# Kernel optimization log

Hardware: AMD Instinct MI355X
Metric: run time of the kernel (lower is better)

## Reference

```python
import jax, jax.numpy as jnp
import numpy as np
from jax import lax

B, L, D, H = 2, 2048, 2048, 16
DH = D // H            # 128 head dim
D_REL = 64             # relevance projection dim (class const)
K = max(1, int(0.25 * L))  # top-K_FRAC tokens per query
NEG_INF = float('-inf')


def setup_inputs() -> dict:
    key = jax.random.key(0)
    ks = jax.random.split(key, 8)
    s = D ** (-0.5)
    return {
        'hidden_states': jax.random.normal(ks[0], (B, L, D), jnp.float32),
        'relevance':     jax.random.normal(ks[1], (B, L, D), jnp.float32),
        # torch nn.Linear weights are [out_features, in_features]
        'W_q_rel': jax.random.normal(ks[2], (D_REL, D), jnp.float32) * s,
        'W_k_rel': jax.random.normal(ks[3], (D_REL, D), jnp.float32) * s,
        'W_q': jax.random.normal(ks[4], (D, D), jnp.float32) * s,
        'W_k': jax.random.normal(ks[5], (D, D), jnp.float32) * s,
        'W_v': jax.random.normal(ks[6], (D, D), jnp.float32) * s,
        'W_o': jax.random.normal(ks[7], (D, D), jnp.float32) * s,
    }


def _rel_scores(relevance, W_q_rel, W_k_rel):
    # low-rank relevance logits, causally masked: [B, L, L]
    q = relevance @ W_q_rel.T   # [B, L, d_rel]
    k = relevance @ W_k_rel.T   # [B, L, d_rel]
    scores = jnp.einsum('bqd,bkd->bqk', q, k) * (D_REL ** -0.5)
    future = jnp.triu(jnp.ones((L, L), dtype=bool), k=1)
    return jnp.where(future[None], NEG_INF, scores)


def _sparse_mask(rel_scores):
    # additive mask [B, 1, L, L]: top-k per query row -> 0.0, else -inf; diag 0.0
    _, topk_idx = lax.top_k(rel_scores, K)            # [B, L, K]
    b = jnp.arange(B)[:, None, None]
    q = jnp.arange(L)[None, :, None]
    mask = jnp.full((B, L, L), NEG_INF, dtype=rel_scores.dtype)
    mask = mask.at[b, q, topk_idx].set(0.0)
    diag = jnp.arange(L)
    mask = mask.at[:, diag, diag].set(0.0)
    return mask[:, None]  # [B, 1, L, L]


def _attention(hidden_states, W_q, W_k, W_v, W_o, add_mask):
    # standard multi-head attention with additive mask (the wrapped frozen attn)
    q = (hidden_states @ W_q.T).reshape(B, L, H, DH)
    k = (hidden_states @ W_k.T).reshape(B, L, H, DH)
    v = (hidden_states @ W_v.T).reshape(B, L, H, DH)
    scores = jnp.einsum('bqhd,bkhd->bhqk', q, k) * (DH ** -0.5)
    scores = scores + add_mask                      # [B, H, L, L]
    p = jax.nn.softmax(scores, axis=-1)
    ctx = jnp.einsum('bhqk,bkhd->bqhd', p, v).reshape(B, L, D)
    return ctx @ W_o.T


def reference(hidden_states, relevance, W_q_rel, W_k_rel, W_q, W_k, W_v, W_o):
    # Phase 1 path (step >= SPARSE_FROM), no external attention_mask:
    # combined = causal(-inf upper-tri) + sparse top-k mask.
    rel = _rel_scores(relevance, W_q_rel, W_k_rel)
    sparse = _sparse_mask(rel)                      # [B, 1, L, L]
    future = jnp.triu(jnp.ones((L, L), dtype=bool), k=1)
    causal = jnp.where(future, NEG_INF, 0.0).astype(hidden_states.dtype)
    combined = causal[None, None] + sparse          # [B, 1, L, L]
    return _attention(hidden_states, W_q, W_k, W_v, W_o, combined)
```

## Files before the change

### kernel.cpp

```cpp
#include <hip/hip_runtime.h>
#include <math.h>
#include <stdint.h>

#define Bb 2
#define Lq 2048
#define Dm 2048
#define Hh 16
#define DH 128
#define DREL 64
#define KTOP 512

#define NEG_INF (-__builtin_huge_valf())

typedef __attribute__((ext_vector_type(8))) short bf16x8;
typedef __attribute__((ext_vector_type(4))) float f32x4;

static __device__ __forceinline__ unsigned short f2bf(float f) {
  unsigned int u = __float_as_uint(f);
  u += 0x7fffu + ((u >> 16) & 1u);
  return (unsigned short)(u >> 16);
}

static __device__ __forceinline__ void gload16(const void* g, void* lds) {
  __builtin_amdgcn_global_load_lds(
      (const __attribute__((address_space(1))) uint32_t*)(uintptr_t)g,
      (__attribute__((address_space(3))) uint32_t*)(uint32_t)(uintptr_t)lds,
      16, 0, 0);
}

__global__ __launch_bounds__(256) void conv_bf16(const float* __restrict__ in,
                                                 unsigned short* __restrict__ out,
                                                 int n8, float scale) {
  const int i = blockIdx.x * 256 + threadIdx.x;
  if (i >= n8) return;
  const float4 f0 = ((const float4*)in)[2 * i];
  const float4 f1 = ((const float4*)in)[2 * i + 1];
  bf16x8 o;
  o[0] = (short)f2bf(f0.x * scale); o[1] = (short)f2bf(f0.y * scale);
  o[2] = (short)f2bf(f0.z * scale); o[3] = (short)f2bf(f0.w * scale);
  o[4] = (short)f2bf(f1.x * scale); o[5] = (short)f2bf(f1.y * scale);
  o[6] = (short)f2bf(f1.z * scale); o[7] = (short)f2bf(f1.w * scale);
  *(bf16x8*)(out + 8 * (size_t)i) = o;
}

template <bool BF16OUT>
__global__ __launch_bounds__(256) void gemm_bf(const unsigned short* __restrict__ A,
                                               const unsigned short* __restrict__ W,
                                               void* __restrict__ Cv,
                                               int M, int N, int Kd) {
  __shared__ unsigned short As[128][32];
  __shared__ unsigned short Bs[128][32];
  const int tid = threadIdx.x;
  const int w = tid >> 6;
  const int lane = tid & 63;
  const int l15 = lane & 15;
  const int quad = lane >> 4;
  const int wm = w >> 1, wn = w & 1;
  const int m0 = blockIdx.y * 128, n0 = blockIdx.x * 128;

  const int srow = lane >> 2;
  const int scol = (lane & 3) * 8;

  const unsigned short* aR0 = A + (size_t)(m0 + w * 32 + srow) * Kd + scol;
  const unsigned short* aR1 = aR0 + (size_t)16 * Kd;
  const unsigned short* bR0 = W + (size_t)(n0 + w * 32 + srow) * Kd + scol;
  const unsigned short* bR1 = bR0 + (size_t)16 * Kd;

  f32x4 acc[4][4];
#pragma unroll
  for (int i = 0; i < 4; ++i)
#pragma unroll
    for (int j = 0; j < 4; ++j) acc[i][j] = (f32x4){0.f, 0.f, 0.f, 0.f};

  for (int k0 = 0; k0 < Kd; k0 += 32) {
    gload16(aR0 + k0, &As[w * 32][0]);
    gload16(aR1 + k0, &As[w * 32 + 16][0]);
    gload16(bR0 + k0, &Bs[w * 32][0]);
    gload16(bR1 + k0, &Bs[w * 32 + 16][0]);
    __syncthreads();

    bf16x8 af[4], bfr[4];
#pragma unroll
    for (int im = 0; im < 4; ++im)
      af[im] = *(const bf16x8*)&As[wm * 64 + im * 16 + l15][quad * 8];
#pragma unroll
    for (int in = 0; in < 4; ++in)
      bfr[in] = *(const bf16x8*)&Bs[wn * 64 + in * 16 + l15][quad * 8];
#pragma unroll
    for (int im = 0; im < 4; ++im)
#pragma unroll
      for (int in = 0; in < 4; ++in)
        acc[im][in] = __builtin_amdgcn_mfma_f32_16x16x32_bf16(af[im], bfr[in], acc[im][in], 0, 0, 0);
    __syncthreads();
  }

#pragma unroll
  for (int im = 0; im < 4; ++im) {
#pragma unroll
    for (int in = 0; in < 4; ++in) {
      const int col = n0 + wn * 64 + in * 16 + l15;
#pragma unroll
      for (int r = 0; r < 4; ++r) {
        const int row = m0 + wm * 64 + im * 16 + quad * 4 + r;
        if (BF16OUT)
          ((unsigned short*)Cv)[(size_t)row * N + col] = f2bf(acc[im][in][r]);
        else
          ((float*)Cv)[(size_t)row * N + col] = acc[im][in][r];
      }
    }
  }
}

#define RKS 8
__global__ __launch_bounds__(256) void relproj(const float* __restrict__ A,
                                               const float* __restrict__ W,
                                               float* __restrict__ part, int M) {
  __shared__ float As[16][128];
  __shared__ float Bs[16][64];
  const int ks = blockIdx.x;
  const int m0 = blockIdx.y * 128;
  const int tid = threadIdx.x;
  const int tx = tid & 15;
  const int ty = tid >> 4;
  const int lr = tid >> 1, lk = (tid & 1) * 8;
  const int wr = tid >> 2, wk = (tid & 3) * 4;

  float acc[8][4];
#pragma unroll
  for (int i = 0; i < 8; ++i)
#pragma unroll
    for (int j = 0; j < 4; ++j) acc[i][j] = 0.f;

  const int k00 = ks * (Dm / RKS);
  for (int k0 = k00; k0 < k00 + Dm / RKS; k0 += 16) {
    {
      const float* ap = A + (size_t)(m0 + lr) * Dm + k0 + lk;
      float4 a0 = *(const float4*)(ap);
      float4 a1 = *(const float4*)(ap + 4);
      As[lk + 0][lr] = a0.x; As[lk + 1][lr] = a0.y;
      As[lk + 2][lr] = a0.z; As[lk + 3][lr] = a0.w;
      As[lk + 4][lr] = a1.x; As[lk + 5][lr] = a1.y;
      As[lk + 6][lr] = a1.z; As[lk + 7][lr] = a1.w;
    }
    {
      const float* bp = W + (size_t)wr * Dm + k0 + wk;
      float4 b0 = *(const float4*)(bp);
      Bs[wk + 0][wr] = b0.x; Bs[wk + 1][wr] = b0.y;
      Bs[wk + 2][wr] = b0.z; Bs[wk + 3][wr] = b0.w;
    }
    __syncthreads();
#pragma unroll
    for (int kk = 0; kk < 16; ++kk) {
      float af[8], bf[4];
#pragma unroll
      for (int i = 0; i < 8; ++i) af[i] = As[kk][ty * 8 + i];
#pragma unroll
      for (int j = 0; j < 4; ++j) bf[j] = Bs[kk][tx * 4 + j];
#pragma unroll
      for (int i = 0; i < 8; ++i)
#pragma unroll
        for (int j = 0; j < 4; ++j) acc[i][j] += af[i] * bf[j];
    }
    __syncthreads();
  }

#pragma unroll
  for (int i = 0; i < 8; ++i) {
    float* pp = part + ((size_t)ks * M + m0 + ty * 8 + i) * DREL + tx * 4;
    *(float4*)pp = make_float4(acc[i][0], acc[i][1], acc[i][2], acc[i][3]);
  }
}

__global__ __launch_bounds__(256) void relreduce(const float* __restrict__ pq,
                                                 const float* __restrict__ pk,
                                                 float* __restrict__ qrel,
                                                 float* __restrict__ krel, int n4) {
  const int i = blockIdx.x * 256 + threadIdx.x;
  if (i >= n4) return;
  float4 sq = make_float4(0, 0, 0, 0), sk = sq;
  for (int s = 0; s < RKS; ++s) {
    float4 a = ((const float4*)pq)[(size_t)s * n4 + i];
    float4 b = ((const float4*)pk)[(size_t)s * n4 + i];
    sq.x += a.x; sq.y += a.y; sq.z += a.z; sq.w += a.w;
    sk.x += b.x; sk.y += b.y; sk.z += b.z; sk.w += b.w;
  }
  ((float4*)qrel)[i] = sq;
  ((float4*)krel)[i] = sk;
}

__global__ __launch_bounds__(256) void relscore(const float* __restrict__ qrel,
                                                const float* __restrict__ krel,
                                                float* __restrict__ S) {
  const int jt = blockIdx.x, qt = blockIdx.y, b = blockIdx.z;
  if (jt > qt) return;
  __shared__ float As[16][128];
  __shared__ float Bs[16][128];
  const int tid = threadIdx.x;
  const int q0 = qt * 128, j0 = jt * 128;
  const int tx = tid & 15, ty = tid >> 4;
  const int lr = tid >> 1, lk = (tid & 1) * 8;
  const float* Ab = qrel + (size_t)b * Lq * DREL;
  const float* Kb = krel + (size_t)b * Lq * DREL;

  float acc[8][8];
#pragma unroll
  for (int i = 0; i < 8; ++i)
#pragma unroll
    for (int j = 0; j < 8; ++j) acc[i][j] = 0.f;

  for (int k0 = 0; k0 < DREL; k0 += 16) {
    {
      const float* ap = Ab + (size_t)(q0 + lr) * DREL + k0 + lk;
      float4 a0 = *(const float4*)(ap);
      float4 a1 = *(const float4*)(ap + 4);
      As[lk + 0][lr] = a0.x; As[lk + 1][lr] = a0.y;
      As[lk + 2][lr] = a0.z; As[lk + 3][lr] = a0.w;
      As[lk + 4][lr] = a1.x; As[lk + 5][lr] = a1.y;
      As[lk + 6][lr] = a1.z; As[lk + 7][lr] = a1.w;
    }
    {
      const float* bp = Kb + (size_t)(j0 + lr) * DREL + k0 + lk;
      float4 b0 = *(const float4*)(bp);
      float4 b1 = *(const float4*)(bp + 4);
      Bs[lk + 0][lr] = b0.x; Bs[lk + 1][lr] = b0.y;
      Bs[lk + 2][lr] = b0.z; Bs[lk + 3][lr] = b0.w;
      Bs[lk + 4][lr] = b1.x; Bs[lk + 5][lr] = b1.y;
      Bs[lk + 6][lr] = b1.z; Bs[lk + 7][lr] = b1.w;
    }
    __syncthreads();
#pragma unroll
    for (int kk = 0; kk < 16; ++kk) {
      float af[8], bf[8];
#pragma unroll
      for (int i = 0; i < 8; ++i) af[i] = As[kk][ty * 8 + i];
#pragma unroll
      for (int j = 0; j < 8; ++j) bf[j] = Bs[kk][tx * 8 + j];
#pragma unroll
      for (int i = 0; i < 8; ++i)
#pragma unroll
        for (int j = 0; j < 8; ++j) acc[i][j] += af[i] * bf[j];
    }
    __syncthreads();
  }

  const float sc = 0.125f;
#pragma unroll
  for (int i = 0; i < 8; ++i) {
    float* cp = S + ((size_t)b * Lq + q0 + ty * 8 + i) * Lq + j0 + tx * 8;
    ((float4*)cp)[0] = make_float4(acc[i][0] * sc, acc[i][1] * sc, acc[i][2] * sc, acc[i][3] * sc);
    ((float4*)cp)[1] = make_float4(acc[i][4] * sc, acc[i][5] * sc, acc[i][6] * sc, acc[i][7] * sc);
  }
}

__global__ __launch_bounds__(256) void relselect(const float* __restrict__ S,
                                                 uint32_t* __restrict__ mask) {
  const int w = threadIdx.x >> 6;
  const int lane = threadIdx.x & 63;
  const int ridx = blockIdx.x * 4 + w;
  const int qi = ridx & (Lq - 1);
  const int n = qi + 1;
  const float* srow = S + (size_t)ridx * Lq;

  uint32_t keys[32];
#pragma unroll
  for (int t = 0; t < 32; ++t) {
    const int j = t * 64 + lane;
    const uint32_t u = __float_as_uint(srow[j]);
    const uint32_t k = (u & 0x80000000u) ? ~u : (u | 0x80000000u);
    keys[t] = (j < n) ? k : 0u;
  }

  uint32_t kth = 0u;
  if (n > KTOP) {
    uint32_t pref = 0u;
    int rem = KTOP;
    for (int bit = 31; bit >= 0; --bit) {
      const uint32_t cand = pref | (1u << bit);
      const uint32_t lim = 1u << bit;
      int c = 0;
#pragma unroll
      for (int t = 0; t < 32; ++t) c += ((keys[t] ^ cand) < lim) ? 1 : 0;
      c += __shfl_xor(c, 1);
      c += __shfl_xor(c, 2);
      c += __shfl_xor(c, 4);
      c += __shfl_xor(c, 8);
      c += __shfl_xor(c, 16);
      c += __shfl_xor(c, 32);
      if (c >= rem) pref = cand;
      else rem -= c;
    }
    kth = pref;
  }

  uint32_t* mrow = mask + (size_t)ridx * (Lq / 32);
#pragma unroll
  for (int t = 0; t < 32; ++t) {
    const int j = t * 64 + lane;
    const bool ok = (j < n) && (keys[t] >= kth || j == qi);
    const unsigned long long bal = __ballot(ok);
    if (lane == 0) {
      mrow[2 * t] = (uint32_t)bal;
      mrow[2 * t + 1] = (uint32_t)(bal >> 32);
    }
  }
}

#define ATQ 128
#define TK 64
__global__ __launch_bounds__(512, 4) void attn_flash3(const unsigned short* __restrict__ qkv,
                                                      const uint32_t* __restrict__ mask,
                                                      unsigned short* __restrict__ ctx) {
  __shared__ unsigned short Ks[2][TK][136];
  __shared__ unsigned short Vt[2][2][64][72];
  __shared__ uint32_t mw[2][ATQ][2];

  const int qt = (blockIdx.z == 0) ? ((Lq / ATQ) - 1 - (int)blockIdx.x) : (int)blockIdx.x;
  const int h = blockIdx.y;
  const int b = blockIdx.z;
  const int tid = threadIdx.x;
  const int w = tid >> 6;
  const int lane = tid & 63;
  const int l15 = lane & 15;
  const int quad = lane >> 4;
  const int q0 = qt * ATQ;
  const int STR = 3 * Dm;

  const unsigned short* kbp = qkv + 2048;
  const unsigned short* vbp = qkv + 4096;

  const int myq = q0 + w * 16 + l15;
  const unsigned short* qrow = qkv + (size_t)(b * Lq + myq) * STR + h * DH;
  bf16x8 bq[4];
#pragma unroll
  for (int kk = 0; kk < 4; ++kk) bq[kk] = *(const bf16x8*)(qrow + kk * 32 + quad * 8);

  f32x4 O[8];
#pragma unroll
  for (int f = 0; f < 8; ++f) O[f] = (f32x4){0.f, 0.f, 0.f, 0.f};
  float l_lane = 0.f;

  const int nt = (q0 + ATQ) / TK;

  const int skey = (tid & 255) >> 2;
  const int scg  = tid & 3;
  const int mq   = (tid & 255) >> 1;
  const int msel = tid & 1;
  const int tv = tid - 256;
  const int vkp = tv & 31;
  const int vdg = (tv >> 5) & 7;
  const int vhalf = vkp >> 4;
  const int vkp16 = vkp & 15;
  const int dwc = ((vkp16 >> 1) & 3) * 4 + (vkp16 >> 3) * 2 + (vkp16 & 1);

  const uint32_t* mrow_base = mask + (size_t)(b * Lq + q0 + mq) * (Lq / 32) + msel;
  const unsigned short* krow_base = kbp + (size_t)(b * Lq + skey) * STR + h * DH + scg * 32;
  const unsigned short* vrow_base = vbp + (size_t)(b * Lq + 2 * vkp) * STR + h * DH + vdg * 16;

  bf16x8 r0, r1, r2, r3;
  uint32_t mreg = 0;

#define LOADREGS(KT)                                                       \
  do {                                                                     \
    const int kbase_ = (KT) * TK;                                          \
    if (tid < 256) {                                                       \
      const unsigned short* kr = krow_base + (size_t)kbase_ * STR;         \
      r0 = *(const bf16x8*)(kr);                                           \
      r1 = *(const bf16x8*)(kr + 8);                                       \
      r2 = *(const bf16x8*)(kr + 16);                                      \
      r3 = *(const bf16x8*)(kr + 24);                                      \
      mreg = mrow_base[(KT) * 2];                                          \
    } else {                                                               \
      const unsigned short* vr = vrow_base + (size_t)kbase_ * STR;         \
      r0 = *(const bf16x8*)(vr);                                           \
      r1 = *(const bf16x8*)(vr + 8);                                       \
      r2 = *(const bf16x8*)(vr + STR);                                     \
      r3 = *(const bf16x8*)(vr + STR + 8);                                 \
    }                                                                      \
  } while (0)

#define WRITELDS(BUF)                                                      \
  do {                                                                     \
    if (tid < 256) {                                                       \
      *(bf16x8*)&Ks[BUF][skey][scg * 32 + 0]  = r0;                        \
      *(bf16x8*)&Ks[BUF][skey][scg * 32 + 8]  = r1;                        \
      *(bf16x8*)&Ks[BUF][skey][scg * 32 + 16] = r2;                        \
      *(bf16x8*)&Ks[BUF][skey][scg * 32 + 24] = r3;                        \
      mw[BUF][mq][msel] = mreg;                                            \
    } else {                                                               \
      _Pragma("unroll") for (int i = 0; i < 8; ++i) {                      \
        const int d = vdg * 16 + i;                                        \
        const uint32_t pk = (uint32_t)(unsigned short)r0[i] |              \
                            ((uint32_t)(unsigned short)r2[i] << 16);       \
        ((uint32_t*)&Vt[BUF][vhalf][d >> 1][0])[(d & 1) * 16 + dwc] = pk;  \
      }                                                                    \
      _Pragma("unroll") for (int i = 0; i < 8; ++i) {                      \
        const int d = vdg * 16 + 8 + i;                                    \
        const uint32_t pk = (uint32_t)(unsigned short)r1[i] |              \
                            ((uint32_t)(unsigned short)r3[i] << 16);       \
        ((uint32_t*)&Vt[BUF][vhalf][d >> 1][0])[(d & 1) * 16 + dwc] = pk;  \
      }                                                                    \
    }                                                                      \
  } while (0)

  LOADREGS(0);
  WRITELDS(0);
  __syncthreads();

  int buf = 0;
  for (int kt = 0; kt < nt; ++kt) {
    const bool more = (kt + 1 < nt);
    if (more) LOADREGS(kt + 1);

    __builtin_amdgcn_s_setprio(1);
#pragma unroll
    for (int hh = 0; hh < 2; ++hh) {
      f32x4 acc0 = (f32x4){0.f, 0.f, 0.f, 0.f};
      f32x4 acc1 = acc0;
#pragma unroll
      for (int kk = 0; kk < 4; ++kk) {
        bf16x8 a0 = *(const bf16x8*)&Ks[buf][hh * 32 + l15][kk * 32 + quad * 8];
        bf16x8 a1 = *(const bf16x8*)&Ks[buf][hh * 32 + 16 + l15][kk * 32 + quad * 8];
        acc0 = __builtin_amdgcn_mfma_f32_16x16x32_bf16(a0, bq[kk], acc0, 0, 0, 0);
        acc1 = __builtin_amdgcn_mfma_f32_16x16x32_bf16(a1, bq[kk], acc1, 0, 0, 0);
      }

      const uint32_t mword = mw[buf][w * 16 + l15][hh];
      bf16x8 bp;
      float ps = 0.f;
#pragma unroll
      for (int r = 0; r < 4; ++r) {
        const float p0 = ((mword >> (quad * 4 + r)) & 1u) ? __builtin_amdgcn_exp2f(acc0[r]) : 0.f;
        const float p1 = ((mword >> (16 + quad * 4 + r)) & 1u) ? __builtin_amdgcn_exp2f(acc1[r]) : 0.f;
        ps += p0 + p1;
        bp[r] = (short)f2bf(p0);
        bp[4 + r] = (short)f2bf(p1);
      }
      l_lane += ps;

#pragma unroll
      for (int f = 0; f < 8; ++f) {
        const int d = f * 16 + l15;
        bf16x8 av = *(const bf16x8*)&Vt[buf][hh][d >> 1][(d & 1) * 32 + quad * 8];
        O[f] = __builtin_amdgcn_mfma_f32_16x16x32_bf16(av, bp, O[f], 0, 0, 0);
      }
    }
    __builtin_amdgcn_s_setprio(0);

    if (more) WRITELDS(buf ^ 1);
    __syncthreads();
    buf ^= 1;
  }
#undef LOADREGS
#undef WRITELDS

  l_lane += __shfl_xor(l_lane, 16);
  l_lane += __shfl_xor(l_lane, 32);
  const float rl = 1.0f / l_lane;

  unsigned short* orow = ctx + ((size_t)(b * Lq + q0 + w * 16 + l15)) * Dm + h * DH;
#pragma unroll
  for (int f = 0; f < 8; ++f) {
    ushort4 o4;
    o4.x = f2bf(O[f][0] * rl);
    o4.y = f2bf(O[f][1] * rl);
    o4.z = f2bf(O[f][2] * rl);
    o4.w = f2bf(O[f][3] * rl);
    *(ushort4*)(orow + f * 16 + quad * 4) = o4;
  }
}

extern "C" void kernel_launch(void* const* d_in, const int* in_sizes, int n_in,
                              void* d_out, int out_size, void* d_ws, size_t ws_size,
                              hipStream_t stream) {
  const float* hs  = (const float*)d_in[0];
  const float* rel = (const float*)d_in[1];
  const float* Wqr = (const float*)d_in[2];
  const float* Wkr = (const float*)d_in[3];
  const float* Wq  = (const float*)d_in[4];
  const float* Wk  = (const float*)d_in[5];
  const float* Wv  = (const float*)d_in[6];
  const float* Wo  = (const float*)d_in[7];
  float* out = (float*)d_out;

  const int M = Bb * Lq;
  const int ND = Dm * Dm;
  char* ws = (char*)d_ws;
  size_t off = 0;
  float* qrel = (float*)(ws + off); off += (size_t)M * DREL * 4;
  float* krel = (float*)(ws + off); off += (size_t)M * DREL * 4;
  uint32_t* maskb = (uint32_t*)(ws + off); off += (size_t)M * (Lq / 32) * 4;
  float* partq = (float*)(ws + off); off += (size_t)RKS * M * DREL * 4;
  float* partk = (float*)(ws + off); off += (size_t)RKS * M * DREL * 4;
  float* Sbuf = (float*)(ws + off);
  unsigned short* hsb  = (unsigned short*)(ws + off); off += (size_t)M * Dm * 2;
  unsigned short* qkvb = (unsigned short*)(ws + off); off += (size_t)M * 3 * Dm * 2;
  unsigned short* ctxb = (unsigned short*)(ws + off); off += (size_t)M * Dm * 2;
  unsigned short* Wqb  = (unsigned short*)(ws + off); off += (size_t)ND * 2;
  unsigned short* Wkb  = (unsigned short*)(ws + off); off += (size_t)ND * 2;
  unsigned short* Wvb  = (unsigned short*)(ws + off); off += (size_t)ND * 2;
  unsigned short* Wob  = (unsigned short*)(ws + off); off += (size_t)ND * 2;

  const dim3 blk(256);
  const int hsN8 = M * Dm / 8;
  const int wN8  = ND / 8;
  const float QSCALE = 0.08838834764831845f * 1.4426950408889634f;

  relproj<<<dim3(RKS, M / 128), blk, 0, stream>>>(rel, Wqr, partq, M);
  relproj<<<dim3(RKS, M / 128), blk, 0, stream>>>(rel, Wkr, partk, M);
  relreduce<<<(M * DREL / 4 + 255) / 256, blk, 0, stream>>>(partq, partk, qrel, krel, M * DREL / 4);
  relscore<<<dim3(Lq / 128, Lq / 128, Bb), blk, 0, stream>>>(qrel, krel, Sbuf);
  relselect<<<M / 4, blk, 0, stream>>>(Sbuf, maskb);

  conv_bf16<<<(hsN8 + 255) / 256, blk, 0, stream>>>(hs, hsb, hsN8, 1.0f);
  conv_bf16<<<(wN8 + 255) / 256, blk, 0, stream>>>(Wq, Wqb, wN8, QSCALE);
  conv_bf16<<<(wN8 + 255) / 256, blk, 0, stream>>>(Wk, Wkb, wN8, 1.0f);
  conv_bf16<<<(wN8 + 255) / 256, blk, 0, stream>>>(Wv, Wvb, wN8, 1.0f);
  conv_bf16<<<(wN8 + 255) / 256, blk, 0, stream>>>(Wo, Wob, wN8, 1.0f);

  gemm_bf<true><<<dim3(3 * Dm / 128, M / 128), blk, 0, stream>>>(hsb, Wqb, qkvb, M, 3 * Dm, Dm);

  attn_flash3<<<dim3(Lq / ATQ, Hh, Bb), dim3(512), 0, stream>>>(qkvb, maskb, ctxb);

  gemm_bf<false><<<dim3(Dm / 128, M / 128), blk, 0, stream>>>(ctxb, Wob, out, M, Dm, Dm);
}
```

Baseline: 524.1 us.

## Replace GEMM with 256x256 double-buffered swizzled tile kernel and merge small launches

Replaces the 128x128 single-buffered bf16 GEMM with a 256x256-tile, 512-thread kernel. The new kernel double-buffers 64-wide K slices in LDS with an XOR swizzle, splits the MFMA work into phases with s_setprio, and remaps workgroup IDs in an XCD-aware order. It also merges the four weight-conversion launches into one and the two relevance-projection launches into one z-indexed launch. The aim is more data reuse per tile, less global-load latency exposure and bank conflicts, and less launch overhead. The cost is more registers and LDS per block, and fewer blocks for the output projection (128 tiles).

```diff
diff --git a/kernel.cpp b/kernel.cpp
--- a/kernel.cpp
+++ b/kernel.cpp
@@ -43,65 +43,153 @@
   *(bf16x8*)(out + 8 * (size_t)i) = o;
 }
 
+__global__ __launch_bounds__(256) void conv_bf16_w4(const float* __restrict__ w0,
+                                                    const float* __restrict__ w1,
+                                                    const float* __restrict__ w2,
+                                                    const float* __restrict__ w3,
+                                                    unsigned short* __restrict__ out,
+                                                    float s0) {
+  const int sel = blockIdx.y;
+  const float* in = (sel == 0) ? w0 : (sel == 1) ? w1 : (sel == 2) ? w2 : w3;
+  const float scale = (sel == 0) ? s0 : 1.0f;
+  const int i = blockIdx.x * 256 + threadIdx.x;
+  const float4 f0 = ((const float4*)in)[2 * i];
+  const float4 f1 = ((const float4*)in)[2 * i + 1];
+  bf16x8 o;
+  o[0] = (short)f2bf(f0.x * scale); o[1] = (short)f2bf(f0.y * scale);
+  o[2] = (short)f2bf(f0.z * scale); o[3] = (short)f2bf(f0.w * scale);
+  o[4] = (short)f2bf(f1.x * scale); o[5] = (short)f2bf(f1.y * scale);
+  o[6] = (short)f2bf(f1.z * scale); o[7] = (short)f2bf(f1.w * scale);
+  *(bf16x8*)(out + (size_t)sel * Dm * Dm + 8 * (size_t)i) = o;
+}
+
 template <bool BF16OUT>
-__global__ __launch_bounds__(256) void gemm_bf(const unsigned short* __restrict__ A,
-                                               const unsigned short* __restrict__ W,
-                                               void* __restrict__ Cv,
-                                               int M, int N, int Kd) {
-  __shared__ unsigned short As[128][32];
-  __shared__ unsigned short Bs[128][32];
+__global__ __launch_bounds__(512, 2) void gemm256(const unsigned short* __restrict__ A,
+                                                  const unsigned short* __restrict__ W,
+                                                  void* __restrict__ Cv,
+                                                  int M, int N, int Kd) {
+  __shared__ unsigned short As[2][2][128][64];
+  __shared__ unsigned short Bs[2][2][128][64];
+
   const int tid = threadIdx.x;
   const int w = tid >> 6;
   const int lane = tid & 63;
   const int l15 = lane & 15;
   const int quad = lane >> 4;
-  const int wm = w >> 1, wn = w & 1;
-  const int m0 = blockIdx.y * 128, n0 = blockIdx.x * 128;
-
-  const int srow = lane >> 2;
-  const int scol = (lane & 3) * 8;
-
-  const unsigned short* aR0 = A + (size_t)(m0 + w * 32 + srow) * Kd + scol;
-  const unsigned short* aR1 = aR0 + (size_t)16 * Kd;
-  const unsigned short* bR0 = W + (size_t)(n0 + w * 32 + srow) * Kd + scol;
-  const unsigned short* bR1 = bR0 + (size_t)16 * Kd;
-
-  f32x4 acc[4][4];
-#pragma unroll
-  for (int i = 0; i < 4; ++i)
+  const int wm = w >> 2;
+  const int wn = w & 3;
+
+  const int gx = N >> 8;
+  const int nwg = (M >> 8) * gx;
+  const int cpx = nwg >> 3;
+  const int bid = (int)blockIdx.x;
+  const int lin = (bid & 7) * cpx + (bid >> 3);
+  const int bx = lin % gx, by = lin / gx;
+  const int m0 = by * 256, n0 = bx * 256;
+
+  const int srow = lane >> 3;
+  const int sslot = (lane & 7) ^ srow;
+  const size_t rowK = (size_t)Kd;
+  const unsigned short* aG0 = A + (size_t)(m0 + w * 8 + srow) * rowK + sslot * 8;
+  const unsigned short* aG1 = aG0 + 64 * rowK;
+  const unsigned short* aG2 = aG0 + 128 * rowK;
+  const unsigned short* aG3 = aG0 + 192 * rowK;
+  const unsigned short* bG0 = W + (size_t)(n0 + w * 8 + srow) * rowK + sslot * 8;
+  const unsigned short* bG1 = bG0 + 64 * rowK;
+  const unsigned short* bG2 = bG0 + 128 * rowK;
+  const unsigned short* bG3 = bG0 + 192 * rowK;
+
+  f32x4 acc[8][4];
+#pragma unroll
+  for (int i = 0; i < 8; ++i)
 #pragma unroll
     for (int j = 0; j < 4; ++j) acc[i][j] = (f32x4){0.f, 0.f, 0.f, 0.f};
 
-  for (int k0 = 0; k0 < Kd; k0 += 32) {
-    gload16(aR0 + k0, &As[w * 32][0]);
-    gload16(aR1 + k0, &As[w * 32 + 16][0]);
-    gload16(bR0 + k0, &Bs[w * 32][0]);
-    gload16(bR1 + k0, &Bs[w * 32 + 16][0]);
+  bf16x8 af[4][2];
+  bf16x8 bfr[2][2];
+  const int swz = (l15 & 7) * 8;
+
+#define STAGE(BUF, T)                                         \
+  do {                                                        \
+    const size_t ko = (size_t)(T) * 64;                       \
+    gload16(aG0 + ko, &As[BUF][0][w * 8][0]);                 \
+    gload16(aG1 + ko, &As[BUF][0][64 + w * 8][0]);            \
+    gload16(aG2 + ko, &As[BUF][1][w * 8][0]);                 \
+    gload16(aG3 + ko, &As[BUF][1][64 + w * 8][0]);            \
+    gload16(bG0 + ko, &Bs[BUF][0][w * 8][0]);                 \
+    gload16(bG1 + ko, &Bs[BUF][0][64 + w * 8][0]);            \
+    gload16(bG2 + ko, &Bs[BUF][1][w * 8][0]);                 \
+    gload16(bG3 + ko, &Bs[BUF][1][64 + w * 8][0]);            \
+  } while (0)
+
+#define LOAD_A(BUF, MH)                                                        \
+  _Pragma("unroll") for (int mi = 0; mi < 4; ++mi)                             \
+    _Pragma("unroll") for (int ks = 0; ks < 2; ++ks)                           \
+      af[mi][ks] = *(const bf16x8*)&As[BUF][wm][(MH) * 64 + mi * 16 + l15]     \
+                                      [(ks * 32 + quad * 8) ^ swz];
+
+#define LOAD_B(BUF, NH)                                                        \
+  _Pragma("unroll") for (int ni = 0; ni < 2; ++ni)                             \
+    _Pragma("unroll") for (int ks = 0; ks < 2; ++ks)                           \
+      bfr[ni][ks] = *(const bf16x8*)&Bs[BUF][wn >> 1]                          \
+          [(wn & 1) * 64 + ((NH) * 2 + ni) * 16 + l15]                         \
+          [(ks * 32 + quad * 8) ^ swz];
+
+#define PHASE_MFMA(MH, NH)                                                     \
+  do {                                                                         \
+    __builtin_amdgcn_s_setprio(1);                                             \
+    _Pragma("unroll") for (int mi = 0; mi < 4; ++mi)                           \
+      _Pragma("unroll") for (int ni = 0; ni < 2; ++ni) {                       \
+        acc[(MH) * 4 + mi][(NH) * 2 + ni] =                                    \
+            __builtin_amdgcn_mfma_f32_16x16x32_bf16(                           \
+                af[mi][0], bfr[ni][0], acc[(MH) * 4 + mi][(NH) * 2 + ni], 0, 0, 0); \
+        acc[(MH) * 4 + mi][(NH) * 2 + ni] =                                    \
+            __builtin_amdgcn_mfma_f32_16x16x32_bf16(                           \
+                af[mi][1], bfr[ni][1], acc[(MH) * 4 + mi][(NH) * 2 + ni], 0, 0, 0); \
+      }                                                                        \
+    __builtin_amdgcn_s_setprio(0);                                             \
+  } while (0)
+
+  STAGE(0, 0);
+  __syncthreads();
+
+  const int nt = Kd >> 6;
+  int buf = 0;
+  for (int t = 0; t < nt; ++t) {
+    if (t + 1 < nt) STAGE(buf ^ 1, t + 1);
+
+    LOAD_A(buf, 0);
+    LOAD_B(buf, 0);
+    PHASE_MFMA(0, 0);
+    __builtin_amdgcn_s_barrier();
+
+    LOAD_B(buf, 1);
+    PHASE_MFMA(0, 1);
+    __builtin_amdgcn_s_barrier();
+
+    LOAD_A(buf, 1);
+    PHASE_MFMA(1, 1);
+    __builtin_amdgcn_s_barrier();
+
+    LOAD_B(buf, 0);
+    PHASE_MFMA(1, 0);
+
     __syncthreads();
-
-    bf16x8 af[4], bfr[4];
-#pragma unroll
-    for (int im = 0; im < 4; ++im)
-      af[im] = *(const bf16x8*)&As[wm * 64 + im * 16 + l15][quad * 8];
-#pragma unroll
-    for (int in = 0; in < 4; ++in)
-      bfr[in] = *(const bf16x8*)&Bs[wn * 64 + in * 16 + l15][quad * 8];
-#pragma unroll
-    for (int im = 0; im < 4; ++im)
-#pragma unroll
-      for (int in = 0; in < 4; ++in)
-        acc[im][in] = __builtin_amdgcn_mfma_f32_16x16x32_bf16(af[im], bfr[in], acc[im][in], 0, 0, 0);
-    __syncthreads();
-  }
-
-#pragma unroll
-  for (int im = 0; im < 4; ++im) {
+    buf ^= 1;
+  }
+#undef STAGE
+#undef LOAD_A
+#undef LOAD_B
+#undef PHASE_MFMA
+
+#pragma unroll
+  for (int im = 0; im < 8; ++im) {
 #pragma unroll
     for (int in = 0; in < 4; ++in) {
       const int col = n0 + wn * 64 + in * 16 + l15;
 #pragma unroll
       for (int r = 0; r < 4; ++r) {
-        const int row = m0 + wm * 64 + im * 16 + quad * 4 + r;
+        const int row = m0 + wm * 128 + im * 16 + quad * 4 + r;
         if (BF16OUT)
           ((unsigned short*)Cv)[(size_t)row * N + col] = f2bf(acc[im][in][r]);
         else
@@ -112,9 +200,13 @@
 }
 
 #define RKS 8
-__global__ __launch_bounds__(256) void relproj(const float* __restrict__ A,
-                                               const float* __restrict__ W,
-                                               float* __restrict__ part, int M) {
+__global__ __launch_bounds__(256) void relproj2(const float* __restrict__ A,
+                                                const float* __restrict__ Wqr,
+                                                const float* __restrict__ Wkr,
+                                                float* __restrict__ partq,
+                                                float* __restrict__ partk, int M) {
+  const float* W = blockIdx.z ? Wkr : Wqr;
+  float* part = blockIdx.z ? partk : partq;
   __shared__ float As[16][128];
   __shared__ float Bs[16][64];
   const int ks = blockIdx.x;
@@ -495,31 +587,25 @@
   unsigned short* hsb  = (unsigned short*)(ws + off); off += (size_t)M * Dm * 2;
   unsigned short* qkvb = (unsigned short*)(ws + off); off += (size_t)M * 3 * Dm * 2;
   unsigned short* ctxb = (unsigned short*)(ws + off); off += (size_t)M * Dm * 2;
-  unsigned short* Wqb  = (unsigned short*)(ws + off); off += (size_t)ND * 2;
-  unsigned short* Wkb  = (unsigned short*)(ws + off); off += (size_t)ND * 2;
-  unsigned short* Wvb  = (unsigned short*)(ws + off); off += (size_t)ND * 2;
-  unsigned short* Wob  = (unsigned short*)(ws + off); off += (size_t)ND * 2;
+  unsigned short* Wqkvo = (unsigned short*)(ws + off); off += (size_t)4 * ND * 2;
 
   const dim3 blk(256);
   const int hsN8 = M * Dm / 8;
-  const int wN8  = ND / 8;
   const float QSCALE = 0.08838834764831845f * 1.4426950408889634f;
 
-  relproj<<<dim3(RKS, M / 128), blk, 0, stream>>>(rel, Wqr, partq, M);
-  relproj<<<dim3(RKS, M / 128), blk, 0, stream>>>(rel, Wkr, partk, M);
+  relproj2<<<dim3(RKS, M / 128, 2), blk, 0, stream>>>(rel, Wqr, Wkr, partq, partk, M);
   relreduce<<<(M * DREL / 4 + 255) / 256, blk, 0, stream>>>(partq, partk, qrel, krel, M * DREL / 4);
   relscore<<<dim3(Lq / 128, Lq / 128, Bb), blk, 0, stream>>>(qrel, krel, Sbuf);
   relselect<<<M / 4, blk, 0, stream>>>(Sbuf, maskb);
 
   conv_bf16<<<(hsN8 + 255) / 256, blk, 0, stream>>>(hs, hsb, hsN8, 1.0f);
-  conv_bf16<<<(wN8 + 255) / 256, blk, 0, stream>>>(Wq, Wqb, wN8, QSCALE);
-  conv_bf16<<<(wN8 + 255) / 256, blk, 0, stream>>>(Wk, Wkb, wN8, 1.0f);
-  conv_bf16<<<(wN8 + 255) / 256, blk, 0, stream>>>(Wv, Wvb, wN8, 1.0f);
-  conv_bf16<<<(wN8 + 255) / 256, blk, 0, stream>>>(Wo, Wob, wN8, 1.0f);
-
-  gemm_bf<true><<<dim3(3 * Dm / 128, M / 128), blk, 0, stream>>>(hsb, Wqb, qkvb, M, 3 * Dm, Dm);
+  conv_bf16_w4<<<dim3(ND / 8 / 256, 4), blk, 0, stream>>>(Wq, Wk, Wv, Wo, Wqkvo, QSCALE);
+
+  gemm256<true><<<dim3((M / 256) * (3 * Dm / 256)), dim3(512), 0, stream>>>(
+      hsb, Wqkvo, qkvb, M, 3 * Dm, Dm);
 
   attn_flash3<<<dim3(Lq / ATQ, Hh, Bb), dim3(512), 0, stream>>>(qkvb, maskb, ctxb);
 
-  gemm_bf<false><<<dim3(Dm / 128, M / 128), blk, 0, stream>>>(ctxb, Wob, out, M, Dm, Dm);
-}
+  gemm256<false><<<dim3((M / 256) * (Dm / 256)), dim3(512), 0, stream>>>(
+      ctxb, Wqkvo + (size_t)3 * ND, out, M, Dm, Dm);
+}
```

Result: faster. 489.8 us (-6.5%).
